# Performance work log

Measured on AMD Instinct MI355X. Metric: run time of the kernel, lower is better.

The kernel has to match this reference:

```python
import jax, jax.numpy as jnp
import numpy as np

N_UPDATE = 3

def _lin(key, fan_in, fan_out):
    s = 1.0 / np.sqrt(fan_in)
    k1, k2 = jax.random.split(key)
    W = jax.random.uniform(k1, (fan_in, fan_out), jnp.float32, -s, s)
    b = jax.random.uniform(k2, (fan_out,), jnp.float32, -s, s)
    return W, b

def setup_inputs() -> dict:
    key = jax.random.key(0)
    ks = jax.random.split(key, 12)
    N, E, F_NODE, F_EDGE, H, L, R, T = 50000, 400000, 16, 16, 32, 64, 128, 1
    inp = {}
    inp["x"] = jax.random.normal(ks[0], (N, F_NODE), jnp.float32)
    inp["edge_index"] = jax.random.randint(ks[1], (E, 2), 0, N)  # [E,2] (src,dst)
    inp["edge_attr"] = jax.random.normal(ks[2], (E, F_EDGE), jnp.float32)
    # edge MLP: F_EDGE -> 64 -> 64 -> H*H
    inp["Wm0"], inp["bm0"] = _lin(ks[3], F_EDGE, L)
    inp["Wm1"], inp["bm1"] = _lin(ks[4], L, L)
    inp["Wm2"], inp["bm2"] = _lin(ks[5], L, H * H)
    # NNConv root weight + bias
    inp["root"], inp["bias"] = _lin(ks[6], H, H)
    # readout i-net: 2H -> R -> T ; j-net: H -> R -> T
    inp["Wi0"], inp["bi0"] = _lin(ks[7], 2 * H, R)
    inp["Wi1"], inp["bi1"] = _lin(ks[8], R, T)
    inp["Wj0"], inp["bj0"] = _lin(ks[9], H, R)
    inp["Wj1"], inp["bj1"] = _lin(ks[10], R, T)
    return inp

def reference(x, edge_index, edge_attr, Wm0, bm0, Wm1, bm1, Wm2, bm2,
              root, bias, Wi0, bi0, Wi1, bi1, Wj0, bj0, Wj1, bj1):
    N = x.shape[0]
    H = root.shape[0]
    # h_0 = [x, zeros] padded to hidden_state_size
    h0 = jnp.concatenate([x, jnp.zeros((N, H - x.shape[1]), x.dtype)], axis=1)
    # edge MLP -> per-edge weight matrices (edge_attr constant across updates)
    e = jax.nn.relu(edge_attr @ Wm0 + bm0)
    e = jax.nn.relu(e @ Wm1 + bm1)
    W = (e @ Wm2 + bm2).reshape(-1, H, H)  # [E, H, H]
    src = edge_index[:, 0]
    dst = edge_index[:, 1]
    h = h0
    for _ in range(N_UPDATE):
        msg = jnp.einsum('eh,eho->eo', h[src], W)              # gather + bmm
        agg = jax.ops.segment_sum(msg, dst, num_segments=N)    # scatter-add
        h = h @ root + bias + agg                              # NNConv root/bias
    # mpnn readout: sum_v sigmoid(i([h_T, h_0])) * j(h_T)
    gate = jax.nn.sigmoid(jax.nn.relu(jnp.concatenate([h, h0], 1) @ Wi0 + bi0) @ Wi1 + bi1)
    val = jax.nn.relu(h @ Wj0 + bj0) @ Wj1 + bj1
    return jnp.sum(gate * val, axis=0)  # [target_size]
```

## Files before the change

### kernel.cpp

```cpp
#include <hip/hip_runtime.h>
#include <stdint.h>

#define N_UPDATE 3
#define HD 32
#define FN 16

typedef unsigned short u16;
typedef __bf16 bf16x8 __attribute__((ext_vector_type(8)));
typedef float f32x4 __attribute__((ext_vector_type(4)));

__device__ __forceinline__ float bf2f(u16 u) {
  union { uint32_t i; float f; } v; v.i = ((uint32_t)u) << 16; return v.f;
}
__device__ __forceinline__ u16 f2bf(float f) {
  union { uint32_t i; float f; } v; v.f = f;
  uint32_t x = v.i;
  return (u16)((x + 0x7fffu + ((x >> 16) & 1u)) >> 16);
}

union frag16 { uint4 v; bf16x8 b; u16 s[8]; };

__global__ void k_zero_i(int* __restrict__ p, int n) {
  int i = blockIdx.x * blockDim.x + threadIdx.x;
  if (i < n) p[i] = 0;
}

__global__ void k_hist2(const int* __restrict__ eidx, int* __restrict__ cntS,
                        int* __restrict__ cntD, int E) {
  int e = blockIdx.x * blockDim.x + threadIdx.x;
  if (e >= E) return;
  int2 sd = ((const int2*)eidx)[e];
  atomicAdd(&cntS[sd.x], 1);
  atomicAdd(&cntD[sd.y], 1);
}

__global__ __launch_bounds__(1024) void k_scan(const int* __restrict__ cnt,
                                               int* __restrict__ out1,
                                               int* __restrict__ out2, int N) {
  __shared__ int sums[1024];
  int chunk = (N + 1023) / 1024;
  int beg = threadIdx.x * chunk;
  int end = beg + chunk; if (end > N) end = N;
  if (beg > N) beg = N;
  int s = 0;
  for (int i = beg; i < end; i++) s += cnt[i];
  sums[threadIdx.x] = s;
  __syncthreads();
  for (int off = 1; off < 1024; off <<= 1) {
    int v = (threadIdx.x >= off) ? sums[threadIdx.x - off] : 0;
    __syncthreads();
    sums[threadIdx.x] += v;
    __syncthreads();
  }
  int run = (threadIdx.x == 0) ? 0 : sums[threadIdx.x - 1];
  for (int i = beg; i < end; i++) {
    out1[i] = run;
    if (out2) out2[i] = run;
    run += cnt[i];
  }
  if (end == N) {
    out1[N] = run;
    if (out2) out2[N] = run;
  }
}

__global__ void k_scatter(const int* __restrict__ eidx, int* __restrict__ ptrS,
                          int* __restrict__ ptrD, int2* __restrict__ spd,
                          int* __restrict__ invp, int E) {
  int e = blockIdx.x * blockDim.x + threadIdx.x;
  if (e >= E) return;
  int2 sd = ((const int2*)eidx)[e];
  int pos = atomicAdd(&ptrS[sd.x], 1);
  int dpos = atomicAdd(&ptrD[sd.y], 1);
  spd[pos] = make_int2(sd.x, dpos);
  invp[e] = pos;
}

__global__ void k_prep_bf(const float* __restrict__ Wm2, uint4* __restrict__ Bf) {
  int t = blockIdx.x;
  int lane = threadIdx.x;
  int col = lane & 15;
  int hg = lane >> 4;
  int p = t >> 6;
  int t2 = t & 63;
  int j2 = t2 * 16 + col;
  int o = p * 16 + (j2 >> 6);
  int k = j2 & 63;
  frag16 f;
#pragma unroll
  for (int jj = 0; jj < 8; jj++) {
    int h = hg * 8 + jj;
    f.s[jj] = f2bf(Wm2[k * 1024 + h * 32 + o]);
  }
  Bf[t * 64 + lane] = f.v;
}

__global__ void k_init_h(const float* __restrict__ x, const float* __restrict__ bm2,
                         float* __restrict__ h, float* __restrict__ hbbuf, int N) {
  int idx = blockIdx.x * blockDim.x + threadIdx.x;
  if (idx >= N * HD) return;
  int n = idx >> 5, o = idx & 31;
  float v = (o < FN) ? x[n * FN + o] : 0.f;
  h[idx] = v;
  float hb = 0.f;
#pragma unroll
  for (int k = 0; k < 32; k++)
    hb = fmaf(__shfl(v, k, 32), bm2[k * 32 + o], hb);
  hbbuf[idx] = hb;
}

__global__ __launch_bounds__(256) void k_edge_mlp(
    const float* __restrict__ ea,
    const float* __restrict__ Wm0, const float* __restrict__ bm0,
    const float* __restrict__ Wm1, const float* __restrict__ bm1,
    const int* __restrict__ invp, u16* __restrict__ ee, int E) {
  int e = blockIdx.x * blockDim.x + threadIdx.x;
  if (e >= E) return;
  float a[16];
  {
    const float4* p = (const float4*)(ea + (size_t)e * 16);
    float4 v0 = p[0], v1 = p[1], v2 = p[2], v3 = p[3];
    a[0]=v0.x; a[1]=v0.y; a[2]=v0.z; a[3]=v0.w;
    a[4]=v1.x; a[5]=v1.y; a[6]=v1.z; a[7]=v1.w;
    a[8]=v2.x; a[9]=v2.y; a[10]=v2.z; a[11]=v2.w;
    a[12]=v3.x; a[13]=v3.y; a[14]=v3.z; a[15]=v3.w;
  }
  float t0[64];
#pragma unroll
  for (int j = 0; j < 64; j++) t0[j] = bm0[j];
#pragma unroll
  for (int k = 0; k < 16; k++) {
    float av = a[k];
#pragma unroll
    for (int j = 0; j < 64; j++) t0[j] = fmaf(av, Wm0[k * 64 + j], t0[j]);
  }
#pragma unroll
  for (int j = 0; j < 64; j++) t0[j] = fmaxf(t0[j], 0.f);

  u16* dst = ee + (size_t)invp[e] * 64;
#pragma unroll
  for (int half = 0; half < 2; half++) {
    float t1[32];
#pragma unroll
    for (int j = 0; j < 32; j++) t1[j] = bm1[half * 32 + j];
#pragma unroll
    for (int k = 0; k < 64; k++) {
      float tv = t0[k];
#pragma unroll
      for (int j = 0; j < 32; j++) t1[j] = fmaf(tv, Wm1[k * 64 + half * 32 + j], t1[j]);
    }
    unsigned int out[16];
#pragma unroll
    for (int j = 0; j < 16; j++) {
      u16 lo = f2bf(fmaxf(t1[2 * j], 0.f));
      u16 hi = f2bf(fmaxf(t1[2 * j + 1], 0.f));
      out[j] = (unsigned int)lo | ((unsigned int)hi << 16);
    }
    uint4* op = (uint4*)(dst + half * 32);
#pragma unroll
    for (int q = 0; q < 4; q++) {
      uint4 w; w.x = out[q*4+0]; w.y = out[q*4+1]; w.z = out[q*4+2]; w.w = out[q*4+3];
      op[q] = w;
    }
  }
}

__global__ __launch_bounds__(256) void k_gemm_G(
    const float* __restrict__ h, const uint4* __restrict__ Bf,
    u16* __restrict__ Gb, int N, int p) {
  int wave = threadIdx.x >> 6;
  int lane = threadIdx.x & 63;
  int n0 = blockIdx.x * 16;
  int row = lane & 15;
  int kg = lane >> 4;

  int nr = n0 + row; if (nr > N - 1) nr = N - 1;
  const float* hr = h + (size_t)nr * HD + kg * 8;
  float4 f0 = *(const float4*)hr;
  float4 f1 = *(const float4*)(hr + 4);
  frag16 a;
  a.s[0] = f2bf(f0.x); a.s[1] = f2bf(f0.y); a.s[2] = f2bf(f0.z); a.s[3] = f2bf(f0.w);
  a.s[4] = f2bf(f1.x); a.s[5] = f2bf(f1.y); a.s[6] = f2bf(f1.z); a.s[7] = f2bf(f1.w);

#pragma unroll
  for (int i = 0; i < 16; i++) {
    int jt = wave * 16 + i;
    frag16 b; b.v = Bf[(p * 64 + jt) * 64 + lane];
    f32x4 acc = {0.f, 0.f, 0.f, 0.f};
    acc = __builtin_amdgcn_mfma_f32_16x16x32_bf16(a.b, b.b, acc, 0, 0, 0);

    int o_l = jt >> 2;
    int k = (jt & 3) * 16 + row;
    int idx = (k >> 3) * 128 + o_l * 8 + (k & 7);
#pragma unroll
    for (int r = 0; r < 4; r++) {
      int n = n0 + kg * 4 + r;
      if (n < N) Gb[(size_t)n * 1024 + idx] = f2bf(acc[r]);
    }
  }
}

__global__ __launch_bounds__(256) void k_msg(
    const u16* __restrict__ Gb, const float* __restrict__ hbbuf,
    const u16* __restrict__ ee, const int2* __restrict__ spd,
    float* __restrict__ msgbuf, int E, int p) {
  int t = blockIdx.x * blockDim.x + threadIdx.x;
  int e = t >> 4;
  int o_l = t & 15;
  if (e >= E) return;
  int2 sp = spd[e];

  float acc = hbbuf[(size_t)sp.x * HD + p * 16 + o_l];

  const uint4* ep = (const uint4*)(ee + (size_t)e * 64);
  const uint4* gp = (const uint4*)(Gb + (size_t)sp.x * 1024);
  frag16 eu[8], gu[8];
#pragma unroll
  for (int q = 0; q < 8; q++) {
    eu[q].v = ep[q];
    gu[q].v = gp[q * 16 + o_l];
  }
#pragma unroll
  for (int k = 0; k < 64; k++) {
    acc = fmaf(bf2f(eu[k >> 3].s[k & 7]), bf2f(gu[k >> 3].s[k & 7]), acc);
  }
  msgbuf[(size_t)sp.y * HD + p * 16 + o_l] = acc;
}

__global__ __launch_bounds__(256) void k_aggupd(
    const float* __restrict__ msgbuf, const int* __restrict__ rowptrD,
    const float* __restrict__ h, const float* __restrict__ root,
    const float* __restrict__ bias, const float* __restrict__ bm2,
    float* __restrict__ hn, float* __restrict__ hbbuf, int N) {
  int t = blockIdx.x * blockDim.x + threadIdx.x;
  int n = t >> 5, o = t & 31;
  if (n >= N) return;
  int jb = rowptrD[n], je = rowptrD[n + 1];
  float s = 0.f;
  for (int j = jb; j < je; j++) s += msgbuf[(size_t)j * HD + o];

  float hv = h[(size_t)n * HD + o];
  float acc = bias[o] + s;
#pragma unroll
  for (int k = 0; k < 32; k++)
    acc = fmaf(__shfl(hv, k, 32), root[k * HD + o], acc);
  hn[(size_t)n * HD + o] = acc;

  float hb = 0.f;
#pragma unroll
  for (int k = 0; k < 32; k++)
    hb = fmaf(__shfl(acc, k, 32), bm2[k * 32 + o], hb);
  hbbuf[(size_t)n * HD + o] = hb;
}

__global__ __launch_bounds__(256) void k_readout(
    const float* __restrict__ h, const float* __restrict__ x,
    const float* __restrict__ Wi0, const float* __restrict__ bi0,
    const float* __restrict__ Wi1, const float* __restrict__ bi1,
    const float* __restrict__ Wj0, const float* __restrict__ bj0,
    const float* __restrict__ Wj1, const float* __restrict__ bj1,
    float* __restrict__ partial, int N) {
  int wid = threadIdx.x >> 6;
  int lane = threadIdx.x & 63;
  int n = blockIdx.x * 4 + wid;
  __shared__ float sred[4];
  float contrib = 0.f;
  if (n < N) {
    float uv;
    if (lane < 32) uv = h[(size_t)n * HD + lane];
    else if (lane < 48) uv = x[(size_t)n * FN + lane - 32];
    else uv = 0.f;

    float g1a = bi0[lane], g1b = bi0[lane + 64];
#pragma unroll
    for (int k = 0; k < 64; k++) {
      float u = __shfl(uv, k, 64);
      g1a = fmaf(u, Wi0[k * 128 + lane], g1a);
      g1b = fmaf(u, Wi0[k * 128 + lane + 64], g1b);
    }
    g1a = fmaxf(g1a, 0.f); g1b = fmaxf(g1b, 0.f);
    float gp = g1a * Wi1[lane] + g1b * Wi1[lane + 64];

    float v1a = bj0[lane], v1b = bj0[lane + 64];
#pragma unroll
    for (int k = 0; k < 32; k++) {
      float hk = __shfl(uv, k, 64);
      v1a = fmaf(hk, Wj0[k * 128 + lane], v1a);
      v1b = fmaf(hk, Wj0[k * 128 + lane + 64], v1b);
    }
    v1a = fmaxf(v1a, 0.f); v1b = fmaxf(v1b, 0.f);
    float vp = v1a * Wj1[lane] + v1b * Wj1[lane + 64];

#pragma unroll
    for (int s = 32; s; s >>= 1) {
      gp += __shfl_xor(gp, s, 64);
      vp += __shfl_xor(vp, s, 64);
    }
    float gate = 1.f / (1.f + __expf(-(gp + bi1[0])));
    float val = vp + bj1[0];
    contrib = gate * val;
  }
  if (lane == 0) sred[wid] = contrib;
  __syncthreads();
  if (threadIdx.x == 0) partial[blockIdx.x] = sred[0] + sred[1] + sred[2] + sred[3];
}

__global__ void k_final(const float* __restrict__ partial, float* __restrict__ out, int P) {
  __shared__ float sm[256];
  float s = 0.f;
  for (int i = threadIdx.x; i < P; i += 256) s += partial[i];
  sm[threadIdx.x] = s;
  __syncthreads();
  for (int st = 128; st; st >>= 1) {
    if ((int)threadIdx.x < st) sm[threadIdx.x] += sm[threadIdx.x + st];
    __syncthreads();
  }
  if (threadIdx.x == 0) out[0] = sm[0];
}

extern "C" void kernel_launch(void* const* d_in, const int* in_sizes, int n_in,
                              void* d_out, int out_size, void* d_ws, size_t ws_size,
                              hipStream_t stream) {
  const float* x    = (const float*)d_in[0];
  const int*   eidx = (const int*)d_in[1];
  const float* ea   = (const float*)d_in[2];
  const float* Wm0  = (const float*)d_in[3];
  const float* bm0  = (const float*)d_in[4];
  const float* Wm1  = (const float*)d_in[5];
  const float* bm1  = (const float*)d_in[6];
  const float* Wm2  = (const float*)d_in[7];
  const float* bm2  = (const float*)d_in[8];
  const float* root = (const float*)d_in[9];
  const float* bias = (const float*)d_in[10];
  const float* Wi0  = (const float*)d_in[11];
  const float* bi0  = (const float*)d_in[12];
  const float* Wi1  = (const float*)d_in[13];
  const float* bi1  = (const float*)d_in[14];
  const float* Wj0  = (const float*)d_in[15];
  const float* bj0  = (const float*)d_in[16];
  const float* Wj1  = (const float*)d_in[17];
  const float* bj1  = (const float*)d_in[18];

  int N = in_sizes[0] / FN;
  int E = in_sizes[1] / 2;
  int nb = (N + 3) / 4;

  auto al = [](size_t b) { return (b + 255) & ~(size_t)255; };
  size_t need = al((size_t)N * 1024 * 2)
              + al((size_t)E * 64 * 2)
              + al((size_t)E * HD * 4)
              + al(128 * 64 * sizeof(uint4))
              + 3 * al((size_t)N * HD * 4)
              + 2 * al((size_t)N * 4)
              + 3 * al(((size_t)N + 1) * 4)
              + al((size_t)E * 8)
              + al((size_t)E * 4)
              + al((size_t)nb * 4);
  if (need > ws_size) return;

  char* ws = (char*)d_ws;
  size_t off = 0;
  auto alloc = [&](size_t bytes) { void* p = ws + off; off += al(bytes); return p; };
  u16*   Gb      = (u16*)alloc((size_t)N * 1024 * 2);
  u16*   ee      = (u16*)alloc((size_t)E * 64 * 2);
  float* msgbuf  = (float*)alloc((size_t)E * HD * 4);
  uint4* Bf      = (uint4*)alloc(128 * 64 * sizeof(uint4));
  float* hA      = (float*)alloc((size_t)N * HD * 4);
  float* hB      = (float*)alloc((size_t)N * HD * 4);
  float* hbbuf   = (float*)alloc((size_t)N * HD * 4);
  int*   cntS    = (int*)alloc((size_t)N * 4);
  int*   cntD    = (int*)alloc((size_t)N * 4);
  int*   ptrS    = (int*)alloc(((size_t)N + 1) * 4);
  int*   rowptrD = (int*)alloc(((size_t)N + 1) * 4);
  int*   ptrD    = (int*)alloc(((size_t)N + 1) * 4);
  int2*  spd     = (int2*)alloc((size_t)E * 8);
  int*   invp    = (int*)alloc((size_t)E * 4);
  float* partial = (float*)alloc((size_t)nb * 4);

  int mt = (N + 15) / 16;
  int ng = (N * HD + 255) / 256;
  int eg = (E + 255) / 256;

  int zn = (int)(((char*)cntD - (char*)cntS) / 4) + N;
  hipLaunchKernelGGL(k_zero_i, dim3((zn + 255) / 256), dim3(256), 0, stream, cntS, zn);
  hipLaunchKernelGGL(k_hist2, dim3(eg), dim3(256), 0, stream, eidx, cntS, cntD, E);
  hipLaunchKernelGGL(k_scan, dim3(1), dim3(1024), 0, stream, cntS, ptrS, (int*)nullptr, N);
  hipLaunchKernelGGL(k_scan, dim3(1), dim3(1024), 0, stream, cntD, rowptrD, ptrD, N);
  hipLaunchKernelGGL(k_scatter, dim3(eg), dim3(256), 0, stream,
                     eidx, ptrS, ptrD, spd, invp, E);

  hipLaunchKernelGGL(k_prep_bf, dim3(128), dim3(64), 0, stream, Wm2, Bf);
  hipLaunchKernelGGL(k_init_h, dim3(ng), dim3(256), 0, stream, x, bm2, hA, hbbuf, N);
  hipLaunchKernelGGL(k_edge_mlp, dim3(eg), dim3(256), 0, stream,
                     ea, Wm0, bm0, Wm1, bm1, invp, ee, E);

  float* hc = hA; float* hn = hB;
  for (int it = 0; it < N_UPDATE; it++) {
    for (int p = 0; p < 2; p++) {
      hipLaunchKernelGGL(k_gemm_G, dim3(mt), dim3(256), 0, stream, hc, Bf, Gb, N, p);
      hipLaunchKernelGGL(k_msg, dim3(((size_t)E * 16 + 255) / 256), dim3(256), 0, stream,
                         Gb, hbbuf, ee, spd, msgbuf, E, p);
    }
    hipLaunchKernelGGL(k_aggupd, dim3(ng), dim3(256), 0, stream,
                       msgbuf, rowptrD, hc, root, bias, bm2, hn, hbbuf, N);
    float* tmp = hc; hc = hn; hn = tmp;
  }

  hipLaunchKernelGGL(k_readout, dim3(nb), dim3(256), 0, stream,
                     hc, x, Wi0, bi0, Wi1, bi1, Wj0, bj0, Wj1, bj1, partial, N);
  hipLaunchKernelGGL(k_final, dim3(1), dim3(256), 0, stream, partial, (float*)d_out, nb);
}
```

Measured before the change: 1.455 ms.

## Split edge MLP across 16 lanes per edge and spread gemm_G tiles over grid

The edge MLP now assigns 16 threads per edge instead of one. Each lane computes 4 of the 64 hidden outputs and gets its inputs through width-16 shuffles, which cuts per-thread register pressure (64-float arrays before) and raises occupancy. The G GEMM kernel moves its 16-iteration per-wave tile loop into a second grid dimension, so each wave does one MFMA tile. This adds parallelism but reloads and reconverts the h fragment 16 times as often, and the edge output writes become 2-byte scalar stores instead of 16-byte vector stores.

```diff
diff --git a/kernel.cpp b/kernel.cpp
--- a/kernel.cpp
+++ b/kernel.cpp
@@ -114,55 +114,44 @@
     const float* __restrict__ Wm0, const float* __restrict__ bm0,
     const float* __restrict__ Wm1, const float* __restrict__ bm1,
     const int* __restrict__ invp, u16* __restrict__ ee, int E) {
-  int e = blockIdx.x * blockDim.x + threadIdx.x;
+  int t = blockIdx.x * blockDim.x + threadIdx.x;
+  int e = t >> 4;
+  int l = t & 15;
   if (e >= E) return;
-  float a[16];
-  {
-    const float4* p = (const float4*)(ea + (size_t)e * 16);
-    float4 v0 = p[0], v1 = p[1], v2 = p[2], v3 = p[3];
-    a[0]=v0.x; a[1]=v0.y; a[2]=v0.z; a[3]=v0.w;
-    a[4]=v1.x; a[5]=v1.y; a[6]=v1.z; a[7]=v1.w;
-    a[8]=v2.x; a[9]=v2.y; a[10]=v2.z; a[11]=v2.w;
-    a[12]=v3.x; a[13]=v3.y; a[14]=v3.z; a[15]=v3.w;
-  }
-  float t0[64];
-#pragma unroll
-  for (int j = 0; j < 64; j++) t0[j] = bm0[j];
+  float aval = ea[(size_t)e * 16 + l];
+
+  float t0r[4];
+#pragma unroll
+  for (int m = 0; m < 4; m++) t0r[m] = bm0[l + 16 * m];
 #pragma unroll
   for (int k = 0; k < 16; k++) {
-    float av = a[k];
-#pragma unroll
-    for (int j = 0; j < 64; j++) t0[j] = fmaf(av, Wm0[k * 64 + j], t0[j]);
-  }
-#pragma unroll
-  for (int j = 0; j < 64; j++) t0[j] = fmaxf(t0[j], 0.f);
+    float av = __shfl(aval, k, 16);
+#pragma unroll
+    for (int m = 0; m < 4; m++)
+      t0r[m] = fmaf(av, Wm0[k * 64 + l + 16 * m], t0r[m]);
+  }
+#pragma unroll
+  for (int m = 0; m < 4; m++) t0r[m] = fmaxf(t0r[m], 0.f);
+
+  float t1r[4];
+#pragma unroll
+  for (int m = 0; m < 4; m++) t1r[m] = bm1[l + 16 * m];
+#pragma unroll
+  for (int km = 0; km < 4; km++) {
+#pragma unroll
+    for (int kl = 0; kl < 16; kl++) {
+      float tv = __shfl(t0r[km], kl, 16);
+      int k = km * 16 + kl;
+#pragma unroll
+      for (int m = 0; m < 4; m++)
+        t1r[m] = fmaf(tv, Wm1[k * 64 + l + 16 * m], t1r[m]);
+    }
+  }
 
   u16* dst = ee + (size_t)invp[e] * 64;
 #pragma unroll
-  for (int half = 0; half < 2; half++) {
-    float t1[32];
-#pragma unroll
-    for (int j = 0; j < 32; j++) t1[j] = bm1[half * 32 + j];
-#pragma unroll
-    for (int k = 0; k < 64; k++) {
-      float tv = t0[k];
-#pragma unroll
-      for (int j = 0; j < 32; j++) t1[j] = fmaf(tv, Wm1[k * 64 + half * 32 + j], t1[j]);
-    }
-    unsigned int out[16];
-#pragma unroll
-    for (int j = 0; j < 16; j++) {
-      u16 lo = f2bf(fmaxf(t1[2 * j], 0.f));
-      u16 hi = f2bf(fmaxf(t1[2 * j + 1], 0.f));
-      out[j] = (unsigned int)lo | ((unsigned int)hi << 16);
-    }
-    uint4* op = (uint4*)(dst + half * 32);
-#pragma unroll
-    for (int q = 0; q < 4; q++) {
-      uint4 w; w.x = out[q*4+0]; w.y = out[q*4+1]; w.z = out[q*4+2]; w.w = out[q*4+3];
-      op[q] = w;
-    }
-  }
+  for (int m = 0; m < 4; m++)
+    dst[l + 16 * m] = f2bf(fmaxf(t1r[m], 0.f));
 }
 
 __global__ __launch_bounds__(256) void k_gemm_G(
@@ -170,6 +159,7 @@
     u16* __restrict__ Gb, int N, int p) {
   int wave = threadIdx.x >> 6;
   int lane = threadIdx.x & 63;
+  int jt = blockIdx.y * 4 + wave;
   int n0 = blockIdx.x * 16;
   int row = lane & 15;
   int kg = lane >> 4;
@@ -182,21 +172,18 @@
   a.s[0] = f2bf(f0.x); a.s[1] = f2bf(f0.y); a.s[2] = f2bf(f0.z); a.s[3] = f2bf(f0.w);
   a.s[4] = f2bf(f1.x); a.s[5] = f2bf(f1.y); a.s[6] = f2bf(f1.z); a.s[7] = f2bf(f1.w);
 
-#pragma unroll
-  for (int i = 0; i < 16; i++) {
-    int jt = wave * 16 + i;
-    frag16 b; b.v = Bf[(p * 64 + jt) * 64 + lane];
-    f32x4 acc = {0.f, 0.f, 0.f, 0.f};
-    acc = __builtin_amdgcn_mfma_f32_16x16x32_bf16(a.b, b.b, acc, 0, 0, 0);
-
-    int o_l = jt >> 2;
-    int k = (jt & 3) * 16 + row;
-    int idx = (k >> 3) * 128 + o_l * 8 + (k & 7);
-#pragma unroll
-    for (int r = 0; r < 4; r++) {
-      int n = n0 + kg * 4 + r;
-      if (n < N) Gb[(size_t)n * 1024 + idx] = f2bf(acc[r]);
-    }
+  frag16 b; b.v = Bf[(p * 64 + jt) * 64 + lane];
+
+  f32x4 acc = {0.f, 0.f, 0.f, 0.f};
+  acc = __builtin_amdgcn_mfma_f32_16x16x32_bf16(a.b, b.b, acc, 0, 0, 0);
+
+  int o_l = jt >> 2;
+  int k = (jt & 3) * 16 + row;
+  int idx = (k >> 3) * 128 + o_l * 8 + (k & 7);
+#pragma unroll
+  for (int r = 0; r < 4; r++) {
+    int n = n0 + kg * 4 + r;
+    if (n < N) Gb[(size_t)n * 1024 + idx] = f2bf(acc[r]);
   }
 }
 
@@ -391,13 +378,13 @@
 
   hipLaunchKernelGGL(k_prep_bf, dim3(128), dim3(64), 0, stream, Wm2, Bf);
   hipLaunchKernelGGL(k_init_h, dim3(ng), dim3(256), 0, stream, x, bm2, hA, hbbuf, N);
-  hipLaunchKernelGGL(k_edge_mlp, dim3(eg), dim3(256), 0, stream,
+  hipLaunchKernelGGL(k_edge_mlp, dim3(((size_t)E * 16 + 255) / 256), dim3(256), 0, stream,
                      ea, Wm0, bm0, Wm1, bm1, invp, ee, E);
 
   float* hc = hA; float* hn = hB;
   for (int it = 0; it < N_UPDATE; it++) {
     for (int p = 0; p < 2; p++) {
-      hipLaunchKernelGGL(k_gemm_G, dim3(mt), dim3(256), 0, stream, hc, Bf, Gb, N, p);
+      hipLaunchKernelGGL(k_gemm_G, dim3(mt, 16), dim3(256), 0, stream, hc, Bf, Gb, N, p);
       hipLaunchKernelGGL(k_msg, dim3(((size_t)E * 16 + 255) / 256), dim3(256), 0, stream,
                          Gb, hbbuf, ee, spd, msgbuf, E, p);
     }
```

Measured after the change: 1.777 ms. +22.1%, slower.
